# Kernel tuning notes

Measured on AMD Instinct MI355X. Metric: run time of the kernel, lower is better.

Reference implementation:

```python
import jax, jax.numpy as jnp
import numpy as np

B, T, H, IN, OUT, HORIZON = 65536, 15, 128, 6, 3, 10
LN_EPS = 1e-5


def _w(k, shape, s=0.08):
    return jax.random.normal(k, shape, jnp.float32) * s


def setup_inputs() -> dict:
    key = jax.random.key(0)
    ks = jax.random.split(key, 16)
    return {
        "x": jax.random.normal(ks[0], (B, T, IN), jnp.float32),
        # encoder layer 0 (input 6 -> 128), PyTorch LSTM gate order i,f,g,o
        "W_ih0": _w(ks[1], (4 * H, IN)), "W_hh0": _w(ks[2], (4 * H, H)), "b0": jnp.zeros((4 * H,), jnp.float32),
        # encoder layer 1 (128 -> 128)
        "W_ih1": _w(ks[3], (4 * H, H)), "W_hh1": _w(ks[4], (4 * H, H)), "b1": jnp.zeros((4 * H,), jnp.float32),
        # decoder LSTM (128 -> 128)
        "W_ihd": _w(ks[5], (4 * H, H)), "W_hhd": _w(ks[6], (4 * H, H)), "bd": jnp.zeros((4 * H,), jnp.float32),
        # step embedding [pred_horizon+1, H]
        "emb": _w(ks[7], (HORIZON + 1, H), 0.5),
        # decoder_input_proj: Linear(3+128 -> 128)
        "Wp": _w(ks[8], (H, OUT + H)), "bp": jnp.zeros((H,), jnp.float32),
        # heads
        "Wm": _w(ks[9], (OUT, H)), "bm": jnp.zeros((OUT,), jnp.float32),
        "Ws": _w(ks[10], (OUT, H)), "bs": jnp.zeros((OUT,), jnp.float32),
        # dec_ln
        "ln_g": jnp.ones((H,), jnp.float32), "ln_b": jnp.zeros((H,), jnp.float32),
    }


def _lstm_cell(h, c, x_t, Wih, Whh, b):
    g = x_t @ Wih.T + h @ Whh.T + b  # [B, 4H]
    i, f, gg, o = jnp.split(g, 4, axis=-1)
    c = jax.nn.sigmoid(f) * c + jax.nn.sigmoid(i) * jnp.tanh(gg)
    h = jax.nn.sigmoid(o) * jnp.tanh(c)
    return h, c


def _run_lstm_layer(seq, Wih, Whh, b):
    # seq: [B, T, D] -> outputs [B, T, H], final (h, c)
    n = seq.shape[0]
    h0 = jnp.zeros((n, H), seq.dtype)
    c0 = jnp.zeros((n, H), seq.dtype)

    def step(carry, xt):
        h, c = carry
        h, c = _lstm_cell(h, c, xt, Wih, Whh, b)
        return (h, c), h

    (h, c), outs = jax.lax.scan(step, (h0, c0), jnp.swapaxes(seq, 0, 1))
    return jnp.swapaxes(outs, 0, 1), h, c


def _layernorm(x, g, b):
    mu = jnp.mean(x, axis=-1, keepdims=True)
    var = jnp.mean(jnp.square(x - mu), axis=-1, keepdims=True)
    return (x - mu) * jax.lax.rsqrt(var + LN_EPS) * g + b


def reference(x, W_ih0, W_hh0, b0, W_ih1, W_hh1, b1, W_ihd, W_hhd, bd, emb, Wp, bp, Wm, bm, Ws, bs, ln_g, ln_b):
    # --- encoder: 2-layer LSTM (eval mode, no dropout) ---
    out0, _, _ = _run_lstm_layer(x, W_ih0, W_hh0, b0)
    _, h_enc, c_enc = _run_lstm_layer(out0, W_ih1, W_hh1, b1)

    prev0 = x[:, -1, :OUT]  # [B, 3]
    n = x.shape[0]

    def dstep(carry, step):
        h, c, prev = carry
        se = jnp.broadcast_to(emb[step], (n, H))
        dec_in = jax.nn.relu(jnp.concatenate([prev, se], axis=-1) @ Wp.T + bp)
        h, c = _lstm_cell(h, c, dec_in, W_ihd, W_hhd, bd)
        feat = _layernorm(h, ln_g, ln_b)
        mu = feat @ Wm.T + bm
        ls = jnp.clip(feat @ Ws.T + bs, -6.0, 3.0)
        prev = jax.lax.stop_gradient(mu)  # mu.detach()
        return (h, c, prev), (mu, ls)

    _, (mus, lss) = jax.lax.scan(dstep, (h_enc, c_enc, prev0), jnp.arange(HORIZON))
    means = jnp.swapaxes(mus, 0, 1)     # [B, HORIZON, 3]
    log_stds = jnp.swapaxes(lss, 0, 1)  # [B, HORIZON, 3]
    return means, log_stds
```

## Files before the change

kernel.cpp:

```cpp
#include <hip/hip_runtime.h>
#include <stdint.h>

typedef __attribute__((ext_vector_type(8))) short short8;
typedef __attribute__((ext_vector_type(4))) float f32x4;

#define NT 15

#define SET0 0
#define SET1 81920
#define SET2 212992
#define SET3 344064
#define PK_TOTAL 346112
#define DD_OFF (PK_TOTAL*2)

__device__ __forceinline__ unsigned short f2bf(float f){
  unsigned int u = __builtin_bit_cast(unsigned int, f);
  u += 0x7fffu + ((u >> 16) & 1u);
  return (unsigned short)(u >> 16);
}
__device__ __forceinline__ float sigf(float x){
  return __builtin_amdgcn_rcpf(1.0f + __expf(-x));
}
__device__ __forceinline__ float tanhf_(float x){
  return 1.0f - 2.0f*__builtin_amdgcn_rcpf(1.0f + __expf(2.0f*x));
}
__device__ __forceinline__ int sidx(int row, int col){
  return row*128 + (col ^ ((row & 7) << 3));
}
__device__ __forceinline__ void BAR(){
  asm volatile("s_waitcnt lgkmcnt(0)" ::: "memory");
  __builtin_amdgcn_s_barrier();
}

__global__ void pack_w(const float* __restrict__ Wih0, const float* __restrict__ Whh0,
                       const float* __restrict__ Wih1, const float* __restrict__ Whh1,
                       const float* __restrict__ Wihd, const float* __restrict__ Whhd,
                       const float* __restrict__ Wm,  const float* __restrict__ Ws,
                       unsigned short* __restrict__ pk)
{
  int idx = blockIdx.x*256 + threadIdx.x;
  if (idx >= PK_TOTAL) return;
  float v = 0.f;
  if (idx >= SET3){
    int e = idx - SET3;
    int j = e & 7, lane = (e >> 3) & 63, kt = e >> 9;
    int n = lane & 15;
    int k = kt*32 + (lane >> 4)*8 + j;
    if (n < 3) v = Wm[n*128 + k];
    else if (n < 6) v = Ws[(n-3)*128 + k];
  } else {
    int set, e;
    if (idx < SET1){ set = 0; e = idx; }
    else if (idx < SET2){ set = 1; e = idx - SET1; }
    else { set = 2; e = idx - SET2; }
    int j = e & 7, lane = (e >> 3) & 63, rest = e >> 9;
    int nf = (set == 0) ? 5 : 8;
    int kt = rest % nf, pair = rest / nf;
    int g = pair & 3, jt = pair >> 2;
    int n = g*128 + jt*16 + (lane & 15);
    int kk = (lane >> 4)*8 + j;
    if (set == 0){
      if (kt < 4) v = Whh0[n*128 + kt*32 + kk];
      else if (kk < 6) v = Wih0[n*6 + kk];
    } else {
      const float* Wi = (set == 1) ? Wih1 : Wihd;
      const float* Wh = (set == 1) ? Whh1 : Whhd;
      v = (kt < 4) ? Wi[n*128 + kt*32 + kk] : Wh[n*128 + (kt-4)*32 + kk];
    }
  }
  pk[idx] = f2bf(v);
}

__global__ void prep_dec(const float* __restrict__ emb, const float* __restrict__ Wp,
                         const float* __restrict__ bp,
                         const float* __restrict__ Wm, const float* __restrict__ Ws,
                         const float* __restrict__ bm, const float* __restrict__ bs,
                         const float* __restrict__ lng, const float* __restrict__ lnb,
                         float* __restrict__ dd)
{
  int idx = blockIdx.x*128 + threadIdx.x;
  if (idx < 1280){
    int s = idx >> 7, j = idx & 127;
    float acc = bp[j];
    for (int k = 0; k < 128; ++k) acc += emb[s*128 + k] * Wp[j*131 + 3 + k];
    dd[idx] = acc;
  } else if (idx < 2048){
    int e = idx - 1280; int o = e >> 7, j = e & 127;
    const float* W = (o < 3) ? (Wm + o*128) : (Ws + (o-3)*128);
    dd[idx] = W[j] * lng[j];
  } else if (idx < 2054){
    int o = idx - 2048;
    const float* W = (o < 3) ? (Wm + o*128) : (Ws + (o-3)*128);
    float a = 0.f;
    for (int k = 0; k < 128; ++k) a += W[k]*lng[k];
    dd[idx] = a;
  } else if (idx < 2060){
    int o = idx - 2054;
    const float* W = (o < 3) ? (Wm + o*128) : (Ws + (o-3)*128);
    float a = (o < 3) ? bm[o] : bs[o-3];
    for (int k = 0; k < 128; ++k) a += W[k]*lnb[k];
    dd[idx] = a;
  }
}

__global__ __launch_bounds__(512, 2)
void traj_main(const float* __restrict__ x,
               const unsigned short* __restrict__ pk,
               const float* __restrict__ dd,
               const float* __restrict__ b0g, const float* __restrict__ b1g,
               const float* __restrict__ bdg,
               const float* __restrict__ Wp,
               float* __restrict__ out)
{
  __shared__ __align__(16) unsigned short hA[2][64*128];
  __shared__ __align__(16) unsigned short hB[2][64*128];
  __shared__ __align__(16) union {
    unsigned short xs[NT*64*8];
    struct { float om[64][30]; float os[64][30]; } o;
  } u2;
  __shared__ __align__(16) struct {
    float sred[8][64][8];
    float prevb[64][4];
  } u;

  const int tid  = threadIdx.x;
  const int w    = tid >> 6;
  const int lane = tid & 63;
  const int lidx = lane & 15;
  const int lgrp = lane >> 4;
  const int col  = w*16 + lidx;
  const int row0 = blockIdx.x * 64;

  for (int i = tid; i < 64*128; i += 512){ hA[1][i] = 0; hB[1][i] = 0; }
  for (int i = tid; i < NT*64*8; i += 512){
    int k8 = i & 7, rt = i >> 3;
    int r = rt & 63, t = rt >> 6;
    u2.xs[i] = (k8 < 6) ? f2bf(x[(size_t)(row0 + r)*90 + t*6 + k8])
                        : (unsigned short)0;
  }

  float b0v[4], b1v[4];
  #pragma unroll
  for (int g = 0; g < 4; ++g){ b0v[g] = b0g[g*128 + col]; b1v[g] = b1g[g*128 + col]; }

  float c0[4][4], c1[4][4];
  #pragma unroll
  for (int m = 0; m < 4; ++m)
    #pragma unroll
    for (int r = 0; r < 4; ++r){ c0[m][r] = 0.f; c1[m][r] = 0.f; }

  __syncthreads();

  const unsigned short* pw0 = pk + SET0 + (w*4)*(5*512) + lane*8;
  const unsigned short* pw1 = pk + SET1 + (w*4)*(8*512) + lane*8;
  const unsigned short* pw2 = pk + SET2 + (w*4)*(8*512) + lane*8;
  const short8 z8 = {0,0,0,0,0,0,0,0};

  #pragma unroll 1
  for (int k = 0; k <= NT; ++k){
    const unsigned short* h0rd = &hA[(k+1)&1][0];
    unsigned short*       h0wr = &hA[k&1][0];
    const unsigned short* h1rd = &hB[k&1][0];
    unsigned short*       h1wr = &hB[(k+1)&1][0];

    if (k < NT){
      f32x4 acc[4][4];
      #pragma unroll
      for (int m = 0; m < 4; ++m)
        #pragma unroll
        for (int g = 0; g < 4; ++g)
          acc[m][g] = (f32x4){b0v[g], b0v[g], b0v[g], b0v[g]};
      #pragma unroll
      for (int kt = 0; kt < 5; ++kt){
        short8 am[4];
        #pragma unroll
        for (int m = 0; m < 4; ++m){
          const int arow = m*16 + lidx;
          if (kt < 4)
            am[m] = *(const short8*)&h0rd[sidx(arow, kt*32 + lgrp*8)];
          else
            am[m] = (lgrp == 0) ? *(const short8*)&u2.xs[(k*64 + arow)*8] : z8;
        }
        #pragma unroll
        for (int g = 0; g < 4; ++g){
          short8 wv = *(const short8*)&pw0[(g*5 + kt)*512];
          #pragma unroll
          for (int m = 0; m < 4; ++m)
            acc[m][g] = __builtin_amdgcn_mfma_f32_16x16x32_bf16(am[m], wv, acc[m][g], 0, 0, 0);
        }
      }
      #pragma unroll
      for (int m = 0; m < 4; ++m)
        #pragma unroll
        for (int r = 0; r < 4; ++r){
          float iv = sigf(acc[m][0][r]);
          float fv = sigf(acc[m][1][r]);
          float gv = tanhf_(acc[m][2][r]);
          float ov = sigf(acc[m][3][r]);
          float c = fv*c0[m][r] + iv*gv;
          c0[m][r] = c;
          h0wr[sidx(m*16 + lgrp*4 + r, col)] = f2bf(ov*tanhf_(c));
        }
    }

    if (k >= 1){
      f32x4 acc[4][4];
      #pragma unroll
      for (int m = 0; m < 4; ++m)
        #pragma unroll
        for (int g = 0; g < 4; ++g)
          acc[m][g] = (f32x4){b1v[g], b1v[g], b1v[g], b1v[g]};
      #pragma unroll
      for (int kt = 0; kt < 8; ++kt){
        short8 am[4];
        #pragma unroll
        for (int m = 0; m < 4; ++m){
          const int arow = m*16 + lidx;
          if (kt < 4)
            am[m] = *(const short8*)&h0rd[sidx(arow, kt*32 + lgrp*8)];
          else
            am[m] = *(const short8*)&h1rd[sidx(arow, (kt-4)*32 + lgrp*8)];
        }
        #pragma unroll
        for (int g = 0; g < 4; ++g){
          short8 wv = *(const short8*)&pw1[(g*8 + kt)*512];
          #pragma unroll
          for (int m = 0; m < 4; ++m)
            acc[m][g] = __builtin_amdgcn_mfma_f32_16x16x32_bf16(am[m], wv, acc[m][g], 0, 0, 0);
        }
      }
      #pragma unroll
      for (int m = 0; m < 4; ++m)
        #pragma unroll
        for (int r = 0; r < 4; ++r){
          float iv = sigf(acc[m][0][r]);
          float fv = sigf(acc[m][1][r]);
          float gv = tanhf_(acc[m][2][r]);
          float ov = sigf(acc[m][3][r]);
          float c = fv*c1[m][r] + iv*gv;
          c1[m][r] = c;
          h1wr[sidx(m*16 + lgrp*4 + r, col)] = f2bf(ov*tanhf_(c));
        }
    }
    BAR();
  }

  const float* dbase = dd;
  const float* hwp   = dd + 1280;
  const float* hbp   = dd + 2048;
  const float* hcp   = dd + 2054;

  const float wpa = Wp[col*131 + 0], wpb = Wp[col*131 + 1], wpc = Wp[col*131 + 2];
  float bdv[4];
  #pragma unroll
  for (int g = 0; g < 4; ++g) bdv[g] = bdg[g*128 + col];
  float hwv[6], hbv[6], hcv[6];
  #pragma unroll
  for (int o = 0; o < 6; ++o){
    hwv[o] = hwp[o*128 + col];
    hbv[o] = hbp[o];
    hcv[o] = hcp[o];
  }

  if (tid < 192){
    int r = tid / 3, o = tid - r*3;
    u.prevb[r][o] = x[(size_t)(row0 + r)*90 + 14*6 + o];
  }
  __syncthreads();

  int hcur = 0, hnew = 1;
  #pragma unroll 1
  for (int s = 0; s < 10; ++s){
    unsigned short* bdin = &hA[0][0];
    const unsigned short* bh = &hB[hcur][0];
    unsigned short* bhn = &hB[hnew][0];

    const float dbs = dbase[s*128 + col];
    #pragma unroll
    for (int m = 0; m < 4; ++m)
      #pragma unroll
      for (int r = 0; r < 4; ++r){
        const int row = m*16 + lgrp*4 + r;
        f32x4 pv = *(const f32x4*)&u.prevb[row][0];
        float v = dbs + pv[0]*wpa + pv[1]*wpb + pv[2]*wpc;
        bdin[sidx(row, col)] = f2bf(v > 0.f ? v : 0.f);
      }
    BAR();

    {
      f32x4 acc[4][4];
      #pragma unroll
      for (int m = 0; m < 4; ++m)
        #pragma unroll
        for (int g = 0; g < 4; ++g)
          acc[m][g] = (f32x4){bdv[g], bdv[g], bdv[g], bdv[g]};
      #pragma unroll
      for (int kt = 0; kt < 8; ++kt){
        short8 am[4];
        #pragma unroll
        for (int m = 0; m < 4; ++m){
          const int arow = m*16 + lidx;
          if (kt < 4)
            am[m] = *(const short8*)&bdin[sidx(arow, kt*32 + lgrp*8)];
          else
            am[m] = *(const short8*)&bh[sidx(arow, (kt-4)*32 + lgrp*8)];
        }
        #pragma unroll
        for (int g = 0; g < 4; ++g){
          short8 wv = *(const short8*)&pw2[(g*8 + kt)*512];
          #pragma unroll
          for (int m = 0; m < 4; ++m)
            acc[m][g] = __builtin_amdgcn_mfma_f32_16x16x32_bf16(am[m], wv, acc[m][g], 0, 0, 0);
        }
      }
      #pragma unroll
      for (int m = 0; m < 4; ++m)
        #pragma unroll
        for (int r = 0; r < 4; ++r){
          float iv = sigf(acc[m][0][r]);
          float fv = sigf(acc[m][1][r]);
          float gv = tanhf_(acc[m][2][r]);
          float ov = sigf(acc[m][3][r]);
          float c = fv*c1[m][r] + iv*gv;
          c1[m][r] = c;
          float h = ov*tanhf_(c);
          const int row = m*16 + lgrp*4 + r;
          bhn[sidx(row, col)] = f2bf(h);
          float vals[8];
          vals[0] = h; vals[1] = h*h;
          #pragma unroll
          for (int o = 0; o < 6; ++o) vals[2+o] = h*hwv[o];
          #pragma unroll
          for (int d = 1; d < 16; d <<= 1)
            #pragma unroll
            for (int kk = 0; kk < 8; ++kk)
              vals[kk] += __shfl_xor(vals[kk], d);
          if (lidx == 0){
            *(f32x4*)&u.sred[w][row][0] = (f32x4){vals[0], vals[1], vals[2], vals[3]};
            *(f32x4*)&u.sred[w][row][4] = (f32x4){vals[4], vals[5], vals[6], vals[7]};
          }
        }
    }
    BAR();

    if (tid < 64){
      float s1 = 0.f, s2 = 0.f;
      float A[6] = {0.f, 0.f, 0.f, 0.f, 0.f, 0.f};
      #pragma unroll
      for (int ww = 0; ww < 8; ++ww){
        f32x4 v0 = *(const f32x4*)&u.sred[ww][tid][0];
        f32x4 v1 = *(const f32x4*)&u.sred[ww][tid][4];
        s1 += v0[0]; s2 += v0[1];
        A[0] += v0[2]; A[1] += v0[3];
        A[2] += v1[0]; A[3] += v1[1]; A[4] += v1[2]; A[5] += v1[3];
      }
      float mu = s1 * (1.f/128.f);
      float var = s2 * (1.f/128.f) - mu*mu;
      float rs = __builtin_amdgcn_rsqf(var + 1e-5f);
      #pragma unroll
      for (int o = 0; o < 3; ++o){
        float v = rs*(A[o] - mu*hbv[o]) + hcv[o];
        u2.o.om[tid][s*3 + o] = v;
        u.prevb[tid][o] = v;
      }
      #pragma unroll
      for (int o = 3; o < 6; ++o){
        float v = rs*(A[o] - mu*hbv[o]) + hcv[o];
        u2.o.os[tid][s*3 + (o-3)] = fminf(fmaxf(v, -6.f), 3.f);
      }
    }
    BAR();
    int tswap = hcur; hcur = hnew; hnew = tswap;
  }

  for (int i = tid; i < 1920; i += 512){
    int r = i / 30, cx = i - r*30;
    out[(size_t)(row0 + r)*30 + cx] = u2.o.om[r][cx];
    out[(size_t)65536*30 + (size_t)(row0 + r)*30 + cx] = u2.o.os[r][cx];
  }
}

extern "C" void kernel_launch(void* const* d_in, const int* in_sizes, int n_in,
                              void* d_out, int out_size, void* d_ws, size_t ws_size,
                              hipStream_t stream)
{
  const float* x    = (const float*)d_in[0];
  const float* Wih0 = (const float*)d_in[1];
  const float* Whh0 = (const float*)d_in[2];
  const float* b0   = (const float*)d_in[3];
  const float* Wih1 = (const float*)d_in[4];
  const float* Whh1 = (const float*)d_in[5];
  const float* b1   = (const float*)d_in[6];
  const float* Wihd = (const float*)d_in[7];
  const float* Whhd = (const float*)d_in[8];
  const float* bd   = (const float*)d_in[9];
  const float* emb  = (const float*)d_in[10];
  const float* Wp   = (const float*)d_in[11];
  const float* bp   = (const float*)d_in[12];
  const float* Wm   = (const float*)d_in[13];
  const float* bm   = (const float*)d_in[14];
  const float* Ws   = (const float*)d_in[15];
  const float* bs   = (const float*)d_in[16];
  const float* lng  = (const float*)d_in[17];
  const float* lnb  = (const float*)d_in[18];

  unsigned short* pkw = (unsigned short*)d_ws;
  float* dd = (float*)((char*)d_ws + DD_OFF);

  pack_w<<<(PK_TOTAL + 255)/256, 256, 0, stream>>>(Wih0, Whh0, Wih1, Whh1,
                                                   Wihd, Whhd, Wm, Ws, pkw);
  prep_dec<<<17, 128, 0, stream>>>(emb, Wp, bp, Wm, Ws, bm, bs, lng, lnb, dd);
  traj_main<<<1024, 512, 0, stream>>>(x, pkw, dd, b0, b1, bd, Wp, (float*)d_out);
}
```

Measured before the change: 2.038 ms.

## Halve rows per block to 32 and give each wave two column tiles

The main kernel now processes 32 batch rows per block with 256 threads (4 waves) instead of 64 rows with 512 threads, launching twice as many blocks. Each wave covers two 16-column slices of every gate, so its MFMA loops iterate over column tiles j2 and two row tiles. LDS is compacted by overlaying the decoder reduction buffers on the layer-0 hidden-state buffer. The goals are a smaller LDS footprint, more resident blocks per CU and less barrier cost per block. In exchange, each weight fragment loaded from global memory feeds only two MFMAs instead of four, which doubles weight traffic per row.

```diff
diff --git a/kernel.cpp b/kernel.cpp
--- a/kernel.cpp
+++ b/kernel.cpp
@@ -5,6 +5,7 @@
 typedef __attribute__((ext_vector_type(4))) float f32x4;
 
 #define NT 15
+#define RW 32
 
 #define SET0 0
 #define SET1 81920
@@ -103,7 +104,7 @@
   }
 }
 
-__global__ __launch_bounds__(512, 2)
+__global__ __launch_bounds__(256)
 void traj_main(const float* __restrict__ x,
                const unsigned short* __restrict__ pk,
                const float* __restrict__ dd,
@@ -112,244 +113,275 @@
                const float* __restrict__ Wp,
                float* __restrict__ out)
 {
-  __shared__ __align__(16) unsigned short hA[2][64*128];
-  __shared__ __align__(16) unsigned short hB[2][64*128];
   __shared__ __align__(16) union {
-    unsigned short xs[NT*64*8];
-    struct { float om[64][30]; float os[64][30]; } o;
+    unsigned short h[2][RW*128];
+    struct {
+      unsigned short pad[RW*128];
+      float sred[4][RW][8];
+      float prevb[RW][4];
+    } d;
+  } uA;
+  __shared__ __align__(16) unsigned short hB[2][RW*128];
+  __shared__ __align__(16) union {
+    unsigned short xs[NT*RW*8];
+    struct { float om[RW][30]; float os[RW][30]; } o;
   } u2;
-  __shared__ __align__(16) struct {
-    float sred[8][64][8];
-    float prevb[64][4];
-  } u;
 
   const int tid  = threadIdx.x;
   const int w    = tid >> 6;
   const int lane = tid & 63;
   const int lidx = lane & 15;
   const int lgrp = lane >> 4;
-  const int col  = w*16 + lidx;
-  const int row0 = blockIdx.x * 64;
-
-  for (int i = tid; i < 64*128; i += 512){ hA[1][i] = 0; hB[1][i] = 0; }
-  for (int i = tid; i < NT*64*8; i += 512){
+  const int row0 = blockIdx.x * RW;
+
+  for (int i = tid; i < RW*128; i += 256){ uA.h[1][i] = 0; hB[1][i] = 0; }
+  for (int i = tid; i < NT*RW*8; i += 256){
     int k8 = i & 7, rt = i >> 3;
-    int r = rt & 63, t = rt >> 6;
+    int r = rt & (RW-1), t = rt >> 5;
     u2.xs[i] = (k8 < 6) ? f2bf(x[(size_t)(row0 + r)*90 + t*6 + k8])
                         : (unsigned short)0;
   }
 
-  float b0v[4], b1v[4];
+  int colv[2]; colv[0] = w*32 + lidx; colv[1] = w*32 + 16 + lidx;
+  float b0v[2][4], b1v[2][4];
   #pragma unroll
-  for (int g = 0; g < 4; ++g){ b0v[g] = b0g[g*128 + col]; b1v[g] = b1g[g*128 + col]; }
-
-  float c0[4][4], c1[4][4];
+  for (int j2 = 0; j2 < 2; ++j2)
+    #pragma unroll
+    for (int g = 0; g < 4; ++g){
+      b0v[j2][g] = b0g[g*128 + colv[j2]];
+      b1v[j2][g] = b1g[g*128 + colv[j2]];
+    }
+
+  float c0[2][2][4], c1[2][2][4];
   #pragma unroll
-  for (int m = 0; m < 4; ++m)
-    #pragma unroll
-    for (int r = 0; r < 4; ++r){ c0[m][r] = 0.f; c1[m][r] = 0.f; }
+  for (int j2 = 0; j2 < 2; ++j2)
+    #pragma unroll
+    for (int m = 0; m < 2; ++m)
+      #pragma unroll
+      for (int r = 0; r < 4; ++r){ c0[j2][m][r] = 0.f; c1[j2][m][r] = 0.f; }
 
   __syncthreads();
 
-  const unsigned short* pw0 = pk + SET0 + (w*4)*(5*512) + lane*8;
-  const unsigned short* pw1 = pk + SET1 + (w*4)*(8*512) + lane*8;
-  const unsigned short* pw2 = pk + SET2 + (w*4)*(8*512) + lane*8;
+  const unsigned short* pw0 = pk + SET0 + (w*8)*(5*512) + lane*8;
+  const unsigned short* pw1 = pk + SET1 + (w*8)*(8*512) + lane*8;
+  const unsigned short* pw2 = pk + SET2 + (w*8)*(8*512) + lane*8;
   const short8 z8 = {0,0,0,0,0,0,0,0};
 
   #pragma unroll 1
   for (int k = 0; k <= NT; ++k){
-    const unsigned short* h0rd = &hA[(k+1)&1][0];
-    unsigned short*       h0wr = &hA[k&1][0];
+    const unsigned short* h0rd = &uA.h[(k+1)&1][0];
+    unsigned short*       h0wr = &uA.h[k&1][0];
     const unsigned short* h1rd = &hB[k&1][0];
     unsigned short*       h1wr = &hB[(k+1)&1][0];
 
     if (k < NT){
-      f32x4 acc[4][4];
-      #pragma unroll
-      for (int m = 0; m < 4; ++m)
+      #pragma unroll
+      for (int j2 = 0; j2 < 2; ++j2){
+        f32x4 acc[2][4];
+        #pragma unroll
+        for (int m = 0; m < 2; ++m)
+          #pragma unroll
+          for (int g = 0; g < 4; ++g)
+            acc[m][g] = (f32x4){b0v[j2][g], b0v[j2][g], b0v[j2][g], b0v[j2][g]};
+        #pragma unroll
+        for (int kt = 0; kt < 5; ++kt){
+          short8 am[2];
+          #pragma unroll
+          for (int m = 0; m < 2; ++m){
+            const int arow = m*16 + lidx;
+            if (kt < 4)
+              am[m] = *(const short8*)&h0rd[sidx(arow, kt*32 + lgrp*8)];
+            else
+              am[m] = (lgrp == 0) ? *(const short8*)&u2.xs[(k*RW + arow)*8] : z8;
+          }
+          #pragma unroll
+          for (int g = 0; g < 4; ++g){
+            short8 wv = *(const short8*)&pw0[((j2*4 + g)*5 + kt)*512];
+            #pragma unroll
+            for (int m = 0; m < 2; ++m)
+              acc[m][g] = __builtin_amdgcn_mfma_f32_16x16x32_bf16(am[m], wv, acc[m][g], 0, 0, 0);
+          }
+        }
+        #pragma unroll
+        for (int m = 0; m < 2; ++m)
+          #pragma unroll
+          for (int r = 0; r < 4; ++r){
+            float iv = sigf(acc[m][0][r]);
+            float fv = sigf(acc[m][1][r]);
+            float gv = tanhf_(acc[m][2][r]);
+            float ov = sigf(acc[m][3][r]);
+            float c = fv*c0[j2][m][r] + iv*gv;
+            c0[j2][m][r] = c;
+            h0wr[sidx(m*16 + lgrp*4 + r, colv[j2])] = f2bf(ov*tanhf_(c));
+          }
+      }
+    }
+
+    if (k >= 1){
+      #pragma unroll
+      for (int j2 = 0; j2 < 2; ++j2){
+        f32x4 acc[2][4];
+        #pragma unroll
+        for (int m = 0; m < 2; ++m)
+          #pragma unroll
+          for (int g = 0; g < 4; ++g)
+            acc[m][g] = (f32x4){b1v[j2][g], b1v[j2][g], b1v[j2][g], b1v[j2][g]};
+        #pragma unroll
+        for (int kt = 0; kt < 8; ++kt){
+          short8 am[2];
+          #pragma unroll
+          for (int m = 0; m < 2; ++m){
+            const int arow = m*16 + lidx;
+            if (kt < 4)
+              am[m] = *(const short8*)&h0rd[sidx(arow, kt*32 + lgrp*8)];
+            else
+              am[m] = *(const short8*)&h1rd[sidx(arow, (kt-4)*32 + lgrp*8)];
+          }
+          #pragma unroll
+          for (int g = 0; g < 4; ++g){
+            short8 wv = *(const short8*)&pw1[((j2*4 + g)*8 + kt)*512];
+            #pragma unroll
+            for (int m = 0; m < 2; ++m)
+              acc[m][g] = __builtin_amdgcn_mfma_f32_16x16x32_bf16(am[m], wv, acc[m][g], 0, 0, 0);
+          }
+        }
+        #pragma unroll
+        for (int m = 0; m < 2; ++m)
+          #pragma unroll
+          for (int r = 0; r < 4; ++r){
+            float iv = sigf(acc[m][0][r]);
+            float fv = sigf(acc[m][1][r]);
+            float gv = tanhf_(acc[m][2][r]);
+            float ov = sigf(acc[m][3][r]);
+            float c = fv*c1[j2][m][r] + iv*gv;
+            c1[j2][m][r] = c;
+            h1wr[sidx(m*16 + lgrp*4 + r, colv[j2])] = f2bf(ov*tanhf_(c));
+          }
+      }
+    }
+    BAR();
+  }
+
+  const float* dbase = dd;
+  const float* hwp   = dd + 1280;
+  const float* hbp   = dd + 2048;
+  const float* hcp   = dd + 2054;
+
+  float wp3[2][3], bdv[2][4], hwv[2][6];
+  #pragma unroll
+  for (int j2 = 0; j2 < 2; ++j2){
+    #pragma unroll
+    for (int o = 0; o < 3; ++o) wp3[j2][o] = Wp[colv[j2]*131 + o];
+    #pragma unroll
+    for (int g = 0; g < 4; ++g) bdv[j2][g] = bdg[g*128 + colv[j2]];
+    #pragma unroll
+    for (int o = 0; o < 6; ++o) hwv[j2][o] = hwp[o*128 + colv[j2]];
+  }
+  float hbv[6], hcv[6];
+  #pragma unroll
+  for (int o = 0; o < 6; ++o){ hbv[o] = hbp[o]; hcv[o] = hcp[o]; }
+
+  if (tid < RW*3){
+    int r = tid / 3, o = tid - r*3;
+    uA.d.prevb[r][o] = x[(size_t)(row0 + r)*90 + 14*6 + o];
+  }
+  __syncthreads();
+
+  int hcur = 0, hnew = 1;
+  #pragma unroll 1
+  for (int s = 0; s < 10; ++s){
+    unsigned short* bdin = &uA.h[0][0];
+    const unsigned short* bh = &hB[hcur][0];
+    unsigned short* bhn = &hB[hnew][0];
+
+    #pragma unroll
+    for (int j2 = 0; j2 < 2; ++j2){
+      const float dbs = dbase[s*128 + colv[j2]];
+      #pragma unroll
+      for (int m = 0; m < 2; ++m)
+        #pragma unroll
+        for (int r = 0; r < 4; ++r){
+          const int row = m*16 + lgrp*4 + r;
+          f32x4 pv = *(const f32x4*)&uA.d.prevb[row][0];
+          float v = dbs + pv[0]*wp3[j2][0] + pv[1]*wp3[j2][1] + pv[2]*wp3[j2][2];
+          bdin[sidx(row, colv[j2])] = f2bf(v > 0.f ? v : 0.f);
+        }
+    }
+    BAR();
+
+    float hreg[2][2][4];
+    #pragma unroll
+    for (int j2 = 0; j2 < 2; ++j2){
+      f32x4 acc[2][4];
+      #pragma unroll
+      for (int m = 0; m < 2; ++m)
         #pragma unroll
         for (int g = 0; g < 4; ++g)
-          acc[m][g] = (f32x4){b0v[g], b0v[g], b0v[g], b0v[g]};
-      #pragma unroll
-      for (int kt = 0; kt < 5; ++kt){
-        short8 am[4];
-        #pragma unroll
-        for (int m = 0; m < 4; ++m){
+          acc[m][g] = (f32x4){bdv[j2][g], bdv[j2][g], bdv[j2][g], bdv[j2][g]};
+      #pragma unroll
+      for (int kt = 0; kt < 8; ++kt){
+        short8 am[2];
+        #pragma unroll
+        for (int m = 0; m < 2; ++m){
           const int arow = m*16 + lidx;
           if (kt < 4)
-            am[m] = *(const short8*)&h0rd[sidx(arow, kt*32 + lgrp*8)];
+            am[m] = *(const short8*)&bdin[sidx(arow, kt*32 + lgrp*8)];
           else
-            am[m] = (lgrp == 0) ? *(const short8*)&u2.xs[(k*64 + arow)*8] : z8;
+            am[m] = *(const short8*)&bh[sidx(arow, (kt-4)*32 + lgrp*8)];
         }
         #pragma unroll
         for (int g = 0; g < 4; ++g){
-          short8 wv = *(const short8*)&pw0[(g*5 + kt)*512];
-          #pragma unroll
-          for (int m = 0; m < 4; ++m)
+          short8 wv = *(const short8*)&pw2[((j2*4 + g)*8 + kt)*512];
+          #pragma unroll
+          for (int m = 0; m < 2; ++m)
             acc[m][g] = __builtin_amdgcn_mfma_f32_16x16x32_bf16(am[m], wv, acc[m][g], 0, 0, 0);
         }
       }
       #pragma unroll
-      for (int m = 0; m < 4; ++m)
+      for (int m = 0; m < 2; ++m)
         #pragma unroll
         for (int r = 0; r < 4; ++r){
           float iv = sigf(acc[m][0][r]);
           float fv = sigf(acc[m][1][r]);
           float gv = tanhf_(acc[m][2][r]);
           float ov = sigf(acc[m][3][r]);
-          float c = fv*c0[m][r] + iv*gv;
-          c0[m][r] = c;
-          h0wr[sidx(m*16 + lgrp*4 + r, col)] = f2bf(ov*tanhf_(c));
-        }
-    }
-
-    if (k >= 1){
-      f32x4 acc[4][4];
-      #pragma unroll
-      for (int m = 0; m < 4; ++m)
-        #pragma unroll
-        for (int g = 0; g < 4; ++g)
-          acc[m][g] = (f32x4){b1v[g], b1v[g], b1v[g], b1v[g]};
-      #pragma unroll
-      for (int kt = 0; kt < 8; ++kt){
-        short8 am[4];
-        #pragma unroll
-        for (int m = 0; m < 4; ++m){
-          const int arow = m*16 + lidx;
-          if (kt < 4)
-            am[m] = *(const short8*)&h0rd[sidx(arow, kt*32 + lgrp*8)];
-          else
-            am[m] = *(const short8*)&h1rd[sidx(arow, (kt-4)*32 + lgrp*8)];
-        }
-        #pragma unroll
-        for (int g = 0; g < 4; ++g){
-          short8 wv = *(const short8*)&pw1[(g*8 + kt)*512];
-          #pragma unroll
-          for (int m = 0; m < 4; ++m)
-            acc[m][g] = __builtin_amdgcn_mfma_f32_16x16x32_bf16(am[m], wv, acc[m][g], 0, 0, 0);
-        }
-      }
-      #pragma unroll
-      for (int m = 0; m < 4; ++m)
-        #pragma unroll
-        for (int r = 0; r < 4; ++r){
-          float iv = sigf(acc[m][0][r]);
-          float fv = sigf(acc[m][1][r]);
-          float gv = tanhf_(acc[m][2][r]);
-          float ov = sigf(acc[m][3][r]);
-          float c = fv*c1[m][r] + iv*gv;
-          c1[m][r] = c;
-          h1wr[sidx(m*16 + lgrp*4 + r, col)] = f2bf(ov*tanhf_(c));
-        }
-    }
+          float c = fv*c1[j2][m][r] + iv*gv;
+          c1[j2][m][r] = c;
+          float h = ov*tanhf_(c);
+          hreg[j2][m][r] = h;
+          bhn[sidx(m*16 + lgrp*4 + r, colv[j2])] = f2bf(h);
+        }
+    }
+    #pragma unroll
+    for (int m = 0; m < 2; ++m)
+      #pragma unroll
+      for (int r = 0; r < 4; ++r){
+        float h0 = hreg[0][m][r], h1 = hreg[1][m][r];
+        float vals[8];
+        vals[0] = h0 + h1;
+        vals[1] = h0*h0 + h1*h1;
+        #pragma unroll
+        for (int o = 0; o < 6; ++o) vals[2+o] = h0*hwv[0][o] + h1*hwv[1][o];
+        #pragma unroll
+        for (int d = 1; d < 16; d <<= 1)
+          #pragma unroll
+          for (int kk = 0; kk < 8; ++kk)
+            vals[kk] += __shfl_xor(vals[kk], d);
+        if (lidx == 0){
+          const int row = m*16 + lgrp*4 + r;
+          *(f32x4*)&uA.d.sred[w][row][0] = (f32x4){vals[0], vals[1], vals[2], vals[3]};
+          *(f32x4*)&uA.d.sred[w][row][4] = (f32x4){vals[4], vals[5], vals[6], vals[7]};
+        }
+      }
     BAR();
-  }
-
-  const float* dbase = dd;
-  const float* hwp   = dd + 1280;
-  const float* hbp   = dd + 2048;
-  const float* hcp   = dd + 2054;
-
-  const float wpa = Wp[col*131 + 0], wpb = Wp[col*131 + 1], wpc = Wp[col*131 + 2];
-  float bdv[4];
-  #pragma unroll
-  for (int g = 0; g < 4; ++g) bdv[g] = bdg[g*128 + col];
-  float hwv[6], hbv[6], hcv[6];
-  #pragma unroll
-  for (int o = 0; o < 6; ++o){
-    hwv[o] = hwp[o*128 + col];
-    hbv[o] = hbp[o];
-    hcv[o] = hcp[o];
-  }
-
-  if (tid < 192){
-    int r = tid / 3, o = tid - r*3;
-    u.prevb[r][o] = x[(size_t)(row0 + r)*90 + 14*6 + o];
-  }
-  __syncthreads();
-
-  int hcur = 0, hnew = 1;
-  #pragma unroll 1
-  for (int s = 0; s < 10; ++s){
-    unsigned short* bdin = &hA[0][0];
-    const unsigned short* bh = &hB[hcur][0];
-    unsigned short* bhn = &hB[hnew][0];
-
-    const float dbs = dbase[s*128 + col];
-    #pragma unroll
-    for (int m = 0; m < 4; ++m)
-      #pragma unroll
-      for (int r = 0; r < 4; ++r){
-        const int row = m*16 + lgrp*4 + r;
-        f32x4 pv = *(const f32x4*)&u.prevb[row][0];
-        float v = dbs + pv[0]*wpa + pv[1]*wpb + pv[2]*wpc;
-        bdin[sidx(row, col)] = f2bf(v > 0.f ? v : 0.f);
-      }
-    BAR();
-
-    {
-      f32x4 acc[4][4];
-      #pragma unroll
-      for (int m = 0; m < 4; ++m)
-        #pragma unroll
-        for (int g = 0; g < 4; ++g)
-          acc[m][g] = (f32x4){bdv[g], bdv[g], bdv[g], bdv[g]};
-      #pragma unroll
-      for (int kt = 0; kt < 8; ++kt){
-        short8 am[4];
-        #pragma unroll
-        for (int m = 0; m < 4; ++m){
-          const int arow = m*16 + lidx;
-          if (kt < 4)
-            am[m] = *(const short8*)&bdin[sidx(arow, kt*32 + lgrp*8)];
-          else
-            am[m] = *(const short8*)&bh[sidx(arow, (kt-4)*32 + lgrp*8)];
-        }
-        #pragma unroll
-        for (int g = 0; g < 4; ++g){
-          short8 wv = *(const short8*)&pw2[(g*8 + kt)*512];
-          #pragma unroll
-          for (int m = 0; m < 4; ++m)
-            acc[m][g] = __builtin_amdgcn_mfma_f32_16x16x32_bf16(am[m], wv, acc[m][g], 0, 0, 0);
-        }
-      }
-      #pragma unroll
-      for (int m = 0; m < 4; ++m)
-        #pragma unroll
-        for (int r = 0; r < 4; ++r){
-          float iv = sigf(acc[m][0][r]);
-          float fv = sigf(acc[m][1][r]);
-          float gv = tanhf_(acc[m][2][r]);
-          float ov = sigf(acc[m][3][r]);
-          float c = fv*c1[m][r] + iv*gv;
-          c1[m][r] = c;
-          float h = ov*tanhf_(c);
-          const int row = m*16 + lgrp*4 + r;
-          bhn[sidx(row, col)] = f2bf(h);
-          float vals[8];
-          vals[0] = h; vals[1] = h*h;
-          #pragma unroll
-          for (int o = 0; o < 6; ++o) vals[2+o] = h*hwv[o];
-          #pragma unroll
-          for (int d = 1; d < 16; d <<= 1)
-            #pragma unroll
-            for (int kk = 0; kk < 8; ++kk)
-              vals[kk] += __shfl_xor(vals[kk], d);
-          if (lidx == 0){
-            *(f32x4*)&u.sred[w][row][0] = (f32x4){vals[0], vals[1], vals[2], vals[3]};
-            *(f32x4*)&u.sred[w][row][4] = (f32x4){vals[4], vals[5], vals[6], vals[7]};
-          }
-        }
-    }
-    BAR();
-
-    if (tid < 64){
+
+    if (tid < RW){
       float s1 = 0.f, s2 = 0.f;
       float A[6] = {0.f, 0.f, 0.f, 0.f, 0.f, 0.f};
       #pragma unroll
-      for (int ww = 0; ww < 8; ++ww){
-        f32x4 v0 = *(const f32x4*)&u.sred[ww][tid][0];
-        f32x4 v1 = *(const f32x4*)&u.sred[ww][tid][4];
+      for (int ww = 0; ww < 4; ++ww){
+        f32x4 v0 = *(const f32x4*)&uA.d.sred[ww][tid][0];
+        f32x4 v1 = *(const f32x4*)&uA.d.sred[ww][tid][4];
         s1 += v0[0]; s2 += v0[1];
         A[0] += v0[2]; A[1] += v0[3];
         A[2] += v1[0]; A[3] += v1[1]; A[4] += v1[2]; A[5] += v1[3];
@@ -361,7 +393,7 @@
       for (int o = 0; o < 3; ++o){
         float v = rs*(A[o] - mu*hbv[o]) + hcv[o];
         u2.o.om[tid][s*3 + o] = v;
-        u.prevb[tid][o] = v;
+        uA.d.prevb[tid][o] = v;
       }
       #pragma unroll
       for (int o = 3; o < 6; ++o){
@@ -373,7 +405,7 @@
     int tswap = hcur; hcur = hnew; hnew = tswap;
   }
 
-  for (int i = tid; i < 1920; i += 512){
+  for (int i = tid; i < RW*30; i += 256){
     int r = i / 30, cx = i - r*30;
     out[(size_t)(row0 + r)*30 + cx] = u2.o.om[r][cx];
     out[(size_t)65536*30 + (size_t)(row0 + r)*30 + cx] = u2.o.os[r][cx];
@@ -410,5 +442,5 @@
   pack_w<<<(PK_TOTAL + 255)/256, 256, 0, stream>>>(Wih0, Whh0, Wih1, Whh1,
                                                    Wihd, Whhd, Wm, Ws, pkw);
   prep_dec<<<17, 128, 0, stream>>>(emb, Wp, bp, Wm, Ws, bm, bs, lng, lnb, dd);
-  traj_main<<<1024, 512, 0, stream>>>(x, pkw, dd, b0, b1, bd, Wp, (float*)d_out);
-}
+  traj_main<<<65536/RW, 256, 0, stream>>>(x, pkw, dd, b0, b1, bd, Wp, (float*)d_out);
+}
```

Result: slower. 2.582 ms (+26.7%).

## Fuse decoder input projection into MFMA A-fragment build and cut barriers per step

Applied to the files above, without the earlier changes.

The decoder loop no longer writes the ReLU input projection to shared memory. Each thread now computes its own A-fragment values directly in registers from a staged Wp slice and step embedding. The layer-norm/head reduction is also done redundantly by every thread for its rows, using a double-buffered sred array, so each decoder step needs one barrier instead of three. This adds redundant ALU work in every wave, drops the min-blocks-per-SM launch bound, and changes the shared-memory layout through a union with the layer-0 h buffer.

```diff
diff --git a/kernel.cpp b/kernel.cpp
--- a/kernel.cpp
+++ b/kernel.cpp
@@ -103,7 +103,7 @@
   }
 }
 
-__global__ __launch_bounds__(512, 2)
+__global__ __launch_bounds__(512)
 void traj_main(const float* __restrict__ x,
                const unsigned short* __restrict__ pk,
                const float* __restrict__ dd,
@@ -112,16 +112,19 @@
                const float* __restrict__ Wp,
                float* __restrict__ out)
 {
-  __shared__ __align__(16) unsigned short hA[2][64*128];
+  __shared__ __align__(16) union {
+    unsigned short h0[2][64*128];
+    struct {
+      float sred[2][8][64][8];
+      float wp3[128][4];
+      float dbl[10][128];
+    } d;
+  } uA;
   __shared__ __align__(16) unsigned short hB[2][64*128];
   __shared__ __align__(16) union {
     unsigned short xs[NT*64*8];
     struct { float om[64][30]; float os[64][30]; } o;
   } u2;
-  __shared__ __align__(16) struct {
-    float sred[8][64][8];
-    float prevb[64][4];
-  } u;
 
   const int tid  = threadIdx.x;
   const int w    = tid >> 6;
@@ -131,7 +134,7 @@
   const int col  = w*16 + lidx;
   const int row0 = blockIdx.x * 64;
 
-  for (int i = tid; i < 64*128; i += 512){ hA[1][i] = 0; hB[1][i] = 0; }
+  for (int i = tid; i < 64*128; i += 512){ uA.h0[1][i] = 0; hB[1][i] = 0; }
   for (int i = tid; i < NT*64*8; i += 512){
     int k8 = i & 7, rt = i >> 3;
     int r = rt & 63, t = rt >> 6;
@@ -158,8 +161,8 @@
 
   #pragma unroll 1
   for (int k = 0; k <= NT; ++k){
-    const unsigned short* h0rd = &hA[(k+1)&1][0];
-    unsigned short*       h0wr = &hA[k&1][0];
+    const unsigned short* h0rd = &uA.h0[(k+1)&1][0];
+    unsigned short*       h0wr = &uA.h0[k&1][0];
     const unsigned short* h1rd = &hB[k&1][0];
     unsigned short*       h1wr = &hB[(k+1)&1][0];
 
@@ -250,7 +253,6 @@
   const float* hbp   = dd + 2048;
   const float* hcp   = dd + 2054;
 
-  const float wpa = Wp[col*131 + 0], wpb = Wp[col*131 + 1], wpc = Wp[col*131 + 2];
   float bdv[4];
   #pragma unroll
   for (int g = 0; g < 4; ++g) bdv[g] = bdg[g*128 + col];
@@ -262,32 +264,65 @@
     hcv[o] = hcp[o];
   }
 
-  if (tid < 192){
-    int r = tid / 3, o = tid - r*3;
-    u.prevb[r][o] = x[(size_t)(row0 + r)*90 + 14*6 + o];
-  }
+  for (int i = tid; i < 128*4; i += 512){
+    int k = i >> 2, o = i & 3;
+    uA.d.wp3[k][o] = (o < 3) ? Wp[k*131 + o] : 0.f;
+  }
+  for (int i = tid; i < 1280; i += 512)
+    uA.d.dbl[i >> 7][i & 127] = dbase[i];
   __syncthreads();
 
   int hcur = 0, hnew = 1;
   #pragma unroll 1
-  for (int s = 0; s < 10; ++s){
-    unsigned short* bdin = &hA[0][0];
-    const unsigned short* bh = &hB[hcur][0];
-    unsigned short* bhn = &hB[hnew][0];
-
-    const float dbs = dbase[s*128 + col];
-    #pragma unroll
-    for (int m = 0; m < 4; ++m)
-      #pragma unroll
-      for (int r = 0; r < 4; ++r){
-        const int row = m*16 + lgrp*4 + r;
-        f32x4 pv = *(const f32x4*)&u.prevb[row][0];
-        float v = dbs + pv[0]*wpa + pv[1]*wpb + pv[2]*wpc;
-        bdin[sidx(row, col)] = f2bf(v > 0.f ? v : 0.f);
+  for (int s = 0; s <= 10; ++s){
+    float prevr[4][3];
+    if (s == 0){
+      #pragma unroll
+      for (int m = 0; m < 4; ++m){
+        const int row = m*16 + lidx;
+        #pragma unroll
+        for (int o = 0; o < 3; ++o)
+          prevr[m][o] = x[(size_t)(row0 + row)*90 + 14*6 + o];
       }
-    BAR();
-
-    {
+    } else {
+      const float (*sr)[64][8] = uA.d.sred[(s + 1) & 1];
+      #pragma unroll
+      for (int m = 0; m < 4; ++m){
+        const int row = m*16 + lidx;
+        float s1 = 0.f, s2 = 0.f;
+        float A0 = 0.f, A1 = 0.f, A2 = 0.f, A3 = 0.f, A4 = 0.f, A5 = 0.f;
+        #pragma unroll
+        for (int ww = 0; ww < 8; ++ww){
+          f32x4 v0 = *(const f32x4*)&sr[ww][row][0];
+          f32x4 v1 = *(const f32x4*)&sr[ww][row][4];
+          s1 += v0[0]; s2 += v0[1]; A0 += v0[2]; A1 += v0[3];
+          A2 += v1[0]; A3 += v1[1]; A4 += v1[2]; A5 += v1[3];
+        }
+        float mu = s1 * (1.f/128.f);
+        float var = s2 * (1.f/128.f) - mu*mu;
+        float rs = __builtin_amdgcn_rsqf(var + 1e-5f);
+        prevr[m][0] = rs*(A0 - mu*hbv[0]) + hcv[0];
+        prevr[m][1] = rs*(A1 - mu*hbv[1]) + hcv[1];
+        prevr[m][2] = rs*(A2 - mu*hbv[2]) + hcv[2];
+        if (w == 0 && lgrp == 0){
+          u2.o.om[row][(s-1)*3 + 0] = prevr[m][0];
+          u2.o.om[row][(s-1)*3 + 1] = prevr[m][1];
+          u2.o.om[row][(s-1)*3 + 2] = prevr[m][2];
+          float q3 = rs*(A3 - mu*hbv[3]) + hcv[3];
+          float q4 = rs*(A4 - mu*hbv[4]) + hcv[4];
+          float q5 = rs*(A5 - mu*hbv[5]) + hcv[5];
+          u2.o.os[row][(s-1)*3 + 0] = fminf(fmaxf(q3, -6.f), 3.f);
+          u2.o.os[row][(s-1)*3 + 1] = fminf(fmaxf(q4, -6.f), 3.f);
+          u2.o.os[row][(s-1)*3 + 2] = fminf(fmaxf(q5, -6.f), 3.f);
+        }
+      }
+    }
+
+    if (s < 10){
+      const unsigned short* bh = &hB[hcur][0];
+      unsigned short* bhn = &hB[hnew][0];
+      float (*srw)[64][8] = uA.d.sred[s & 1];
+
       f32x4 acc[4][4];
       #pragma unroll
       for (int m = 0; m < 4; ++m)
@@ -297,13 +332,30 @@
       #pragma unroll
       for (int kt = 0; kt < 8; ++kt){
         short8 am[4];
-        #pragma unroll
-        for (int m = 0; m < 4; ++m){
-          const int arow = m*16 + lidx;
-          if (kt < 4)
-            am[m] = *(const short8*)&bdin[sidx(arow, kt*32 + lgrp*8)];
-          else
-            am[m] = *(const short8*)&bh[sidx(arow, (kt-4)*32 + lgrp*8)];
+        if (kt < 4){
+          const int k0 = kt*32 + lgrp*8;
+          f32x4 db0 = *(const f32x4*)&uA.d.dbl[s][k0];
+          f32x4 db1 = *(const f32x4*)&uA.d.dbl[s][k0 + 4];
+          f32x4 wpv[8];
+          #pragma unroll
+          for (int j = 0; j < 8; ++j)
+            wpv[j] = *(const f32x4*)&uA.d.wp3[k0 + j][0];
+          #pragma unroll
+          for (int m = 0; m < 4; ++m){
+            short8 a;
+            #pragma unroll
+            for (int j = 0; j < 8; ++j){
+              float db = (j < 4) ? db0[j] : db1[j-4];
+              float v = db + prevr[m][0]*wpv[j][0] + prevr[m][1]*wpv[j][1]
+                           + prevr[m][2]*wpv[j][2];
+              a[j] = (short)f2bf(v > 0.f ? v : 0.f);
+            }
+            am[m] = a;
+          }
+        } else {
+          #pragma unroll
+          for (int m = 0; m < 4; ++m)
+            am[m] = *(const short8*)&bh[sidx(m*16 + lidx, (kt-4)*32 + lgrp*8)];
         }
         #pragma unroll
         for (int g = 0; g < 4; ++g){
@@ -336,43 +388,16 @@
             for (int kk = 0; kk < 8; ++kk)
               vals[kk] += __shfl_xor(vals[kk], d);
           if (lidx == 0){
-            *(f32x4*)&u.sred[w][row][0] = (f32x4){vals[0], vals[1], vals[2], vals[3]};
-            *(f32x4*)&u.sred[w][row][4] = (f32x4){vals[4], vals[5], vals[6], vals[7]};
+            *(f32x4*)&srw[w][row][0] = (f32x4){vals[0], vals[1], vals[2], vals[3]};
+            *(f32x4*)&srw[w][row][4] = (f32x4){vals[4], vals[5], vals[6], vals[7]};
           }
         }
+      BAR();
+      int tswap = hcur; hcur = hnew; hnew = tswap;
     }
-    BAR();
-
-    if (tid < 64){
-      float s1 = 0.f, s2 = 0.f;
-      float A[6] = {0.f, 0.f, 0.f, 0.f, 0.f, 0.f};
-      #pragma unroll
-      for (int ww = 0; ww < 8; ++ww){
-        f32x4 v0 = *(const f32x4*)&u.sred[ww][tid][0];
-        f32x4 v1 = *(const f32x4*)&u.sred[ww][tid][4];
-        s1 += v0[0]; s2 += v0[1];
-        A[0] += v0[2]; A[1] += v0[3];
-        A[2] += v1[0]; A[3] += v1[1]; A[4] += v1[2]; A[5] += v1[3];
-      }
-      float mu = s1 * (1.f/128.f);
-      float var = s2 * (1.f/128.f) - mu*mu;
-      float rs = __builtin_amdgcn_rsqf(var + 1e-5f);
-      #pragma unroll
-      for (int o = 0; o < 3; ++o){
-        float v = rs*(A[o] - mu*hbv[o]) + hcv[o];
-        u2.o.om[tid][s*3 + o] = v;
-        u.prevb[tid][o] = v;
-      }
-      #pragma unroll
-      for (int o = 3; o < 6; ++o){
-        float v = rs*(A[o] - mu*hbv[o]) + hcv[o];
-        u2.o.os[tid][s*3 + (o-3)] = fminf(fmaxf(v, -6.f), 3.f);
-      }
-    }
-    BAR();
-    int tswap = hcur; hcur = hnew; hnew = tswap;
-  }
-
+  }
+
+  __syncthreads();
   for (int i = tid; i < 1920; i += 512){
     int r = i / 30, cx = i - r*30;
     out[(size_t)(row0 + r)*30 + cx] = u2.o.om[r][cx];
```

Measured after the change: 2.005 ms (median of 2 runs). About the same (-1.6%).
